# Performance work log

Hardware: AMD Instinct MI355X
Metric: run time of the kernel (lower is better)

Reference implementation:

```python
import jax, jax.numpy as jnp
import numpy as np

B, T, D, H, V = 512, 128, 1024, 1024, 256
STEPS = 26  # batch_max_length (25) + 1


def setup_inputs() -> dict:
    key = jax.random.key(0)
    ks = jax.random.split(key, 12)
    s = lambda *sh: 1.0 / np.sqrt(sh[-1])
    inp = {
        "batch_H": jax.random.normal(ks[0], (B, T, D), dtype=jnp.float32),
        "text": jax.random.randint(ks[1], (B, STEPS), 0, V, dtype=jnp.int64),
        # AttentionCell params
        "i2h_w": jax.random.normal(ks[2], (H, D), dtype=jnp.float32) * s(H, D),
        "h2h_w": jax.random.normal(ks[3], (H, H), dtype=jnp.float32) * s(H, H),
        "h2h_b": jnp.zeros((H,), dtype=jnp.float32),
        "score_w": jax.random.normal(ks[4], (1, H), dtype=jnp.float32) * s(1, H),
        # LSTMCell params (input = context[D] ++ onehot[V])
        "W_ih": jax.random.normal(ks[5], (4 * H, D + V), dtype=jnp.float32) * s(4 * H, D + V),
        "W_hh": jax.random.normal(ks[6], (4 * H, H), dtype=jnp.float32) * s(4 * H, H),
        "b_ih": jnp.zeros((4 * H,), dtype=jnp.float32),
        "b_hh": jnp.zeros((4 * H,), dtype=jnp.float32),
        # generator
        "gen_w": jax.random.normal(ks[7], (V, H), dtype=jnp.float32) * s(V, H),
        "gen_b": jnp.zeros((V,), dtype=jnp.float32),
    }
    return inp


def reference(batch_H, text, i2h_w, h2h_w, h2h_b, score_w, W_ih, W_hh, b_ih, b_hh, gen_w, gen_b):
    # proj_H = i2h(batch_H): step-invariant, hoisted out of the loop (same math)
    proj_H = jnp.einsum("btd,hd->bth", batch_H, i2h_w)  # [B,T,H]
    dtype = batch_H.dtype

    def step(carry, tok):
        h, c = carry
        # Bahdanau additive attention
        proj_h = h @ h2h_w.T + h2h_b                       # [B,H]
        e = jnp.tanh(proj_H + proj_h[:, None, :]) @ score_w[0]  # [B,T]
        alpha = jax.nn.softmax(e, axis=1)                   # [B,T]
        context = jnp.einsum("bt,btd->bd", alpha, batch_H)  # [B,D]
        x = jnp.concatenate([context, jax.nn.one_hot(tok, V, dtype=dtype)], axis=1)
        # LSTMCell (torch gate order: i, f, g, o)
        gates = x @ W_ih.T + b_ih + h @ W_hh.T + b_hh       # [B,4H]
        i_g, f_g, g_g, o_g = jnp.split(gates, 4, axis=1)
        c_new = jax.nn.sigmoid(f_g) * c + jax.nn.sigmoid(i_g) * jnp.tanh(g_g)
        h_new = jax.nn.sigmoid(o_g) * jnp.tanh(c_new)
        return (h_new, c_new), h_new

    h0 = jnp.zeros((B, H), dtype=dtype)
    c0 = jnp.zeros((B, H), dtype=dtype)
    tokens = jnp.swapaxes(text[:, :STEPS], 0, 1)            # [STEPS,B]
    _, out_hid = jax.lax.scan(step, (h0, c0), tokens)       # [STEPS,B,H]
    out_hid = jnp.swapaxes(out_hid, 0, 1)                   # [B,STEPS,H]
    logits = jnp.einsum("bsh,vh->bsv", out_hid, gen_w) + gen_b
    return logits  # [B, STEPS, V]
```

## Files before the change

### kernel.cpp

```cpp
#include <hip/hip_runtime.h>
#include <hip/hip_fp16.h>

#define BB 512
#define TT 128
#define DD 1024
#define HH 1024
#define VV 256
#define SS 26

typedef _Float16 half8 __attribute__((ext_vector_type(8)));
typedef _Float16 half4 __attribute__((ext_vector_type(4)));
typedef float f32x4 __attribute__((ext_vector_type(4)));

__device__ __forceinline__ float tanh_fast(float x) {
    float ex = __expf(2.f * x);
    return 1.f - 2.f * __builtin_amdgcn_rcpf(ex + 1.f);
}
__device__ __forceinline__ float sigmoid_fast(float x) {
    return __builtin_amdgcn_rcpf(1.f + __expf(-x));
}

__global__ void cvt_f32_to_f16_v4(const float* __restrict__ src,
                                  _Float16* __restrict__ dst, long n4) {
    long i = (long)blockIdx.x * blockDim.x + threadIdx.x;
    long stride = (long)gridDim.x * blockDim.x;
    for (; i < n4; i += stride) {
        float4 v = ((const float4*)src)[i];
        half4 h;
        h[0] = (_Float16)v.x; h[1] = (_Float16)v.y;
        h[2] = (_Float16)v.z; h[3] = (_Float16)v.w;
        ((half4*)dst)[i] = h;
    }
}

__global__ void build_wcatp(const float* __restrict__ W_ih,
                            const float* __restrict__ W_hh,
                            _Float16* __restrict__ wcatp) {
    int idx = blockIdx.x * 256 + threadIdx.x;
    int c = idx >> 11;
    int k = idx & 2047;
    int g = c >> 6, q = (c >> 4) & 3, jl = c & 15;
    int row = q * 1024 + g * 16 + jl;
    float v = (k < 1024) ? W_ih[(size_t)row * 1280 + k]
                         : W_hh[(size_t)row * 1024 + (k - 1024)];
    wcatp[idx] = (_Float16)v;
}

__global__ void build_onehT(const float* __restrict__ W_ih,
                            float* __restrict__ onehT) {
    int idx = blockIdx.x * 256 + threadIdx.x;
    int v = idx >> 12;
    int g = idx & 4095;
    onehT[idx] = W_ih[(size_t)g * 1280 + 1024 + v];
}

__global__ void build_bsum(const float* __restrict__ b_ih,
                           const float* __restrict__ b_hh,
                           float* __restrict__ bsum) {
    int i = blockIdx.x * 256 + threadIdx.x;
    bsum[i] = b_ih[i] + b_hh[i];
}

template <int MODE, int SWZ>
__global__ __launch_bounds__(256) void gemm_bt(
    const _Float16* __restrict__ A, int lda,
    const _Float16* __restrict__ B, int ldb,
    void* __restrict__ Cp, int ldc, int K, const float* __restrict__ bias) {
    __shared__ __align__(16) _Float16 As[128 * 32];
    __shared__ __align__(16) _Float16 Bs[128 * 32];

    int bx = blockIdx.x, by = blockIdx.y;
    if (SWZ) {
        int nx = gridDim.x;
        int bid = by * nx + bx;
        int xcd = bid & 7;
        int local = bid >> 3;
        int rows_per_xcd = gridDim.y >> 3;
        bx = local % nx;
        by = xcd * rows_per_xcd + local / nx;
    }
    const int tid  = threadIdx.x;
    const int lane = tid & 63;
    const int wid  = tid >> 6;
    const int wm   = wid >> 1;
    const int wn   = wid & 1;
    const int m0 = by * 128;
    const int n0 = bx * 128;

    f32x4 acc[4][4];
#pragma unroll
    for (int i = 0; i < 4; ++i)
#pragma unroll
        for (int j = 0; j < 4; ++j)
            acc[i][j] = (f32x4){0.f, 0.f, 0.f, 0.f};

    const int row0 = tid >> 2;
    const int ch0  = tid & 3;
    const _Float16* a0 = A + (size_t)(m0 + row0) * lda + ch0 * 8;
    const _Float16* a1 = A + (size_t)(m0 + row0 + 64) * lda + ch0 * 8;
    const _Float16* b0 = B + (size_t)(n0 + row0) * ldb + ch0 * 8;
    const _Float16* b1 = B + (size_t)(n0 + row0 + 64) * ldb + ch0 * 8;
    _Float16* sa0 = As + row0 * 32 + ch0 * 8;
    _Float16* sa1 = As + (row0 + 64) * 32 + ch0 * 8;
    _Float16* sb0 = Bs + row0 * 32 + ch0 * 8;
    _Float16* sb1 = Bs + (row0 + 64) * 32 + ch0 * 8;

    const int la = lane & 15;
    const int kc = (lane >> 4) * 8;

    for (int k0 = 0; k0 < K; k0 += 32) {
        uint4 va0 = *(const uint4*)(a0 + k0);
        uint4 va1 = *(const uint4*)(a1 + k0);
        uint4 vb0 = *(const uint4*)(b0 + k0);
        uint4 vb1 = *(const uint4*)(b1 + k0);
        __syncthreads();
        *(uint4*)sa0 = va0;
        *(uint4*)sa1 = va1;
        *(uint4*)sb0 = vb0;
        *(uint4*)sb1 = vb1;
        __syncthreads();

        half8 af[4], bf[4];
#pragma unroll
        for (int mt = 0; mt < 4; ++mt)
            af[mt] = *(const half8*)(As + (wm * 64 + mt * 16 + la) * 32 + kc);
#pragma unroll
        for (int nt = 0; nt < 4; ++nt)
            bf[nt] = *(const half8*)(Bs + (wn * 64 + nt * 16 + la) * 32 + kc);
#pragma unroll
        for (int mt = 0; mt < 4; ++mt)
#pragma unroll
            for (int nt = 0; nt < 4; ++nt)
                acc[mt][nt] = __builtin_amdgcn_mfma_f32_16x16x32_f16(
                    af[mt], bf[nt], acc[mt][nt], 0, 0, 0);
    }

#pragma unroll
    for (int mt = 0; mt < 4; ++mt) {
#pragma unroll
        for (int nt = 0; nt < 4; ++nt) {
            int gn = n0 + wn * 64 + nt * 16 + la;
            float bv = bias ? bias[gn] : 0.f;
#pragma unroll
            for (int r = 0; r < 4; ++r) {
                int gm = m0 + wm * 64 + mt * 16 + (lane >> 4) * 4 + r;
                float v = acc[mt][nt][r] + bv;
                if (MODE == 1) {
                    ((_Float16*)Cp)[(size_t)gm * ldc + gn] = (_Float16)v;
                } else {
                    int s = gm >> 9;
                    int b = gm & 511;
                    ((float*)Cp)[((size_t)b * SS + s) * VV + gn] = v;
                }
            }
        }
    }
}

#define GEMM64_CORE(A, lda, B, ldb, K)                                        \
    __shared__ __align__(16) _Float16 As[64 * 32];                            \
    __shared__ __align__(16) _Float16 Bs[128 * 32];                           \
    const int tid  = threadIdx.x;                                             \
    const int lane = tid & 63;                                                \
    const int wid  = tid >> 6;                                                \
    const int wm   = wid >> 1;                                                \
    const int wn   = wid & 1;                                                 \
    const int m0 = blockIdx.y * 64;                                           \
    const int n0 = blockIdx.x * 128;                                          \
    f32x4 acc[2][4];                                                          \
    _Pragma("unroll") for (int i = 0; i < 2; ++i)                             \
        _Pragma("unroll") for (int j = 0; j < 4; ++j)                         \
            acc[i][j] = (f32x4){0.f, 0.f, 0.f, 0.f};                          \
    const int row0 = tid >> 2;                                                \
    const int ch0  = tid & 3;                                                 \
    const _Float16* ag = A + (size_t)(m0 + row0) * lda + ch0 * 8;             \
    const _Float16* bg0 = B + (size_t)(n0 + row0) * ldb + ch0 * 8;            \
    const _Float16* bg1 = B + (size_t)(n0 + row0 + 64) * ldb + ch0 * 8;       \
    _Float16* sa  = As + row0 * 32 + ch0 * 8;                                 \
    _Float16* sb0 = Bs + row0 * 32 + ch0 * 8;                                 \
    _Float16* sb1 = Bs + (row0 + 64) * 32 + ch0 * 8;                          \
    const int la = lane & 15;                                                 \
    const int kc = (lane >> 4) * 8;                                           \
    for (int k0 = 0; k0 < K; k0 += 32) {                                      \
        uint4 va  = *(const uint4*)(ag + k0);                                 \
        uint4 vb0 = *(const uint4*)(bg0 + k0);                                \
        uint4 vb1 = *(const uint4*)(bg1 + k0);                                \
        __syncthreads();                                                      \
        *(uint4*)sa  = va;                                                    \
        *(uint4*)sb0 = vb0;                                                   \
        *(uint4*)sb1 = vb1;                                                   \
        __syncthreads();                                                      \
        half8 af[2], bf[4];                                                   \
        _Pragma("unroll") for (int mt = 0; mt < 2; ++mt)                      \
            af[mt] = *(const half8*)(As + (wm * 32 + mt * 16 + la) * 32 + kc);\
        _Pragma("unroll") for (int nt = 0; nt < 4; ++nt)                      \
            bf[nt] = *(const half8*)(Bs + (wn * 64 + nt * 16 + la) * 32 + kc);\
        _Pragma("unroll") for (int mt = 0; mt < 2; ++mt)                      \
            _Pragma("unroll") for (int nt = 0; nt < 4; ++nt)                  \
                acc[mt][nt] = __builtin_amdgcn_mfma_f32_16x16x32_f16(         \
                    af[mt], bf[nt], acc[mt][nt], 0, 0, 0);                    \
    }

__global__ __launch_bounds__(256) void gemm64_f32(
    const _Float16* __restrict__ A, int lda,
    const _Float16* __restrict__ B, int ldb,
    float* __restrict__ C, int ldc, int K, const float* __restrict__ bias) {
    GEMM64_CORE(A, lda, B, ldb, K)
#pragma unroll
    for (int mt = 0; mt < 2; ++mt)
#pragma unroll
        for (int nt = 0; nt < 4; ++nt) {
            int gn = n0 + wn * 64 + nt * 16 + la;
            float bv = bias[gn];
#pragma unroll
            for (int r = 0; r < 4; ++r) {
                int gm = m0 + wm * 32 + mt * 16 + (lane >> 4) * 4 + r;
                C[(size_t)gm * ldc + gn] = acc[mt][nt][r] + bv;
            }
        }
}

__global__ __launch_bounds__(256) void gemm_gates(
    const _Float16* __restrict__ A,
    const _Float16* __restrict__ B,
    const float* __restrict__ bsum,
    const float* __restrict__ onehT,
    const int* __restrict__ text,
    int step,
    float* __restrict__ c,
    _Float16* __restrict__ acat,
    _Float16* __restrict__ hid) {
    GEMM64_CORE(A, 2048, B, 2048, 2048)
    const int quad = lane >> 4;
    const int jb = (n0 >> 2) + wn * 16 + la;
    float bs[4];
#pragma unroll
    for (int q = 0; q < 4; ++q) bs[q] = bsum[q * 1024 + jb];
#pragma unroll
    for (int mt = 0; mt < 2; ++mt) {
#pragma unroll
        for (int r = 0; r < 4; ++r) {
            int b = m0 + wm * 32 + mt * 16 + quad * 4 + r;
            int tok = text[b * SS + step];
            const float* orow = onehT + (size_t)tok * 4096;
            float ig = acc[mt][0][r] + bs[0] + orow[jb];
            float fg = acc[mt][1][r] + bs[1] + orow[1024 + jb];
            float gg = acc[mt][2][r] + bs[2] + orow[2048 + jb];
            float og = acc[mt][3][r] + bs[3] + orow[3072 + jb];
            size_t ci = (size_t)b * 1024 + jb;
            float cn = sigmoid_fast(fg) * c[ci] + sigmoid_fast(ig) * tanh_fast(gg);
            float hn = sigmoid_fast(og) * tanh_fast(cn);
            c[ci] = cn;
            _Float16 h16 = (_Float16)hn;
            acat[(size_t)b * 2048 + 1024 + jb] = h16;
            hid[((size_t)step * BB + b) * HH + jb] = h16;
        }
    }
}

__global__ __launch_bounds__(256) void attn_kernel(
    const _Float16* __restrict__ pH,
    const _Float16* __restrict__ bh,
    const float* __restrict__ ph,
    const float* __restrict__ sw,
    _Float16* __restrict__ acat) {
    __shared__ float e_s[TT];
    __shared__ float al_s[TT];

    const int b = blockIdx.x;
    const int tid = threadIdx.x;
    const int lane = tid & 63;
    const int wv = tid >> 6;

    float phr[16], swr[16];
    const float4* ph4 = (const float4*)(ph + (size_t)b * HH + lane * 16);
    const float4* sw4 = (const float4*)(sw + lane * 16);
#pragma unroll
    for (int q = 0; q < 4; ++q) {
        float4 t1 = ph4[q];
        phr[q * 4 + 0] = t1.x; phr[q * 4 + 1] = t1.y;
        phr[q * 4 + 2] = t1.z; phr[q * 4 + 3] = t1.w;
        float4 t2 = sw4[q];
        swr[q * 4 + 0] = t2.x; swr[q * 4 + 1] = t2.y;
        swr[q * 4 + 2] = t2.z; swr[q * 4 + 3] = t2.w;
    }

    const _Float16* pHb = pH + (size_t)b * TT * HH + lane * 16;
    for (int tt = 0; tt < 32; ++tt) {
        int t = wv * 32 + tt;
        half8 p0 = *(const half8*)(pHb + (size_t)t * HH);
        half8 p1 = *(const half8*)(pHb + (size_t)t * HH + 8);
        float acc = 0.f;
#pragma unroll
        for (int k = 0; k < 8; ++k)
            acc += tanh_fast((float)p0[k] + phr[k]) * swr[k];
#pragma unroll
        for (int k = 0; k < 8; ++k)
            acc += tanh_fast((float)p1[k] + phr[8 + k]) * swr[8 + k];
#pragma unroll
        for (int off = 32; off > 0; off >>= 1) acc += __shfl_xor(acc, off, 64);
        if (lane == 0) e_s[t] = acc;
    }
    __syncthreads();

    if (tid < TT) {
        float m = -1e30f;
        for (int t = 0; t < TT; ++t) m = fmaxf(m, e_s[t]);
        float s = 0.f;
        for (int t = 0; t < TT; ++t) s += __expf(e_s[t] - m);
        al_s[tid] = __expf(e_s[tid] - m) / s;
    }
    __syncthreads();

    const _Float16* bhb = bh + (size_t)b * TT * DD + tid * 4;
    float c0 = 0.f, c1 = 0.f, c2 = 0.f, c3 = 0.f;
#pragma unroll 4
    for (int t = 0; t < TT; ++t) {
        float a = al_s[t];
        half4 v = *(const half4*)(bhb + (size_t)t * DD);
        c0 += a * (float)v[0];
        c1 += a * (float)v[1];
        c2 += a * (float)v[2];
        c3 += a * (float)v[3];
    }
    half4 o;
    o[0] = (_Float16)c0; o[1] = (_Float16)c1;
    o[2] = (_Float16)c2; o[3] = (_Float16)c3;
    *(half4*)(acat + (size_t)b * 2048 + tid * 4) = o;
}

extern "C" void kernel_launch(void* const* d_in, const int* in_sizes, int n_in,
                              void* d_out, int out_size, void* d_ws, size_t ws_size,
                              hipStream_t stream) {
    const float* batch_H = (const float*)d_in[0];
    const int*   text    = (const int*)d_in[1];
    const float* i2h_w   = (const float*)d_in[2];
    const float* h2h_w   = (const float*)d_in[3];
    const float* h2h_b   = (const float*)d_in[4];
    const float* score_w = (const float*)d_in[5];
    const float* W_ih    = (const float*)d_in[6];
    const float* W_hh    = (const float*)d_in[7];
    const float* b_ih    = (const float*)d_in[8];
    const float* b_hh    = (const float*)d_in[9];
    const float* gen_w   = (const float*)d_in[10];
    const float* gen_b   = (const float*)d_in[11];
    float* out = (float*)d_out;

    char* ws = (char*)d_ws;
    size_t off = 0;
    auto carve = [&](size_t bytes) -> void* {
        void* p = ws + off;
        off += (bytes + 255) & ~(size_t)255;
        return p;
    };
    _Float16* bh16   = (_Float16*)carve((size_t)BB * TT * DD * 2);
    _Float16* pH16   = (_Float16*)carve((size_t)BB * TT * HH * 2);
    _Float16* wi2h16 = (_Float16*)carve((size_t)HH * DD * 2);
    _Float16* wh2h16 = (_Float16*)carve((size_t)HH * HH * 2);
    _Float16* wcatp  = (_Float16*)carve((size_t)4 * HH * 2048 * 2);
    _Float16* wgen16 = (_Float16*)carve((size_t)VV * HH * 2);
    float*    onehT  = (float*)carve((size_t)VV * 4 * HH * 4);
    float*    bsum   = (float*)carve((size_t)4 * HH * 4);
    _Float16* acat   = (_Float16*)carve((size_t)BB * 2048 * 2);
    float*    ph_f   = (float*)carve((size_t)BB * HH * 4);
    float*    c_f    = (float*)carve((size_t)BB * HH * 4);
    _Float16* hid16  = (_Float16*)carve((size_t)SS * BB * HH * 2);

    const dim3 blk(256);

    cvt_f32_to_f16_v4<<<dim3(16384), blk, 0, stream>>>(batch_H, bh16, (long)BB * TT * DD / 4);
    cvt_f32_to_f16_v4<<<dim3(1024), blk, 0, stream>>>(i2h_w, wi2h16, (long)HH * DD / 4);
    cvt_f32_to_f16_v4<<<dim3(1024), blk, 0, stream>>>(h2h_w, wh2h16, (long)HH * HH / 4);
    cvt_f32_to_f16_v4<<<dim3(256), blk, 0, stream>>>(gen_w, wgen16, (long)VV * HH / 4);
    build_wcatp<<<dim3(4 * HH * 2048 / 256), blk, 0, stream>>>(W_ih, W_hh, wcatp);
    build_onehT<<<dim3(VV * 4 * HH / 256), blk, 0, stream>>>(W_ih, onehT);
    build_bsum<<<dim3(16), blk, 0, stream>>>(b_ih, b_hh, bsum);
    hipMemsetAsync(acat, 0, (size_t)BB * 2048 * 2, stream);
    hipMemsetAsync(c_f, 0, (size_t)BB * HH * 4, stream);

    gemm_bt<1, 1><<<dim3(HH / 128, BB * TT / 128), blk, 0, stream>>>(
        bh16, DD, wi2h16, DD, pH16, HH, DD, nullptr);

    for (int s = 0; s < SS; ++s) {
        gemm64_f32<<<dim3(HH / 128, BB / 64), blk, 0, stream>>>(
            acat + 1024, 2048, wh2h16, HH, ph_f, HH, HH, h2h_b);

        attn_kernel<<<dim3(BB), blk, 0, stream>>>(pH16, bh16, ph_f, score_w, acat);

        gemm_gates<<<dim3(4 * HH / 128, BB / 64), blk, 0, stream>>>(
            acat, wcatp, bsum, onehT, text, s, c_f, acat, hid16);
    }

    gemm_bt<2, 0><<<dim3(VV / 128, SS * BB / 128), blk, 0, stream>>>(
        hid16, HH, wgen16, HH, out, VV, HH, gen_b);
}
```

Measured before the change: 3.920 ms.

## Use direct global-to-LDS loads in GEMMs and widen attention to 512 threads

```diff
diff --git a/kernel.cpp b/kernel.cpp
--- a/kernel.cpp
+++ b/kernel.cpp
@@ -11,6 +11,12 @@
 typedef _Float16 half8 __attribute__((ext_vector_type(8)));
 typedef _Float16 half4 __attribute__((ext_vector_type(4)));
 typedef float f32x4 __attribute__((ext_vector_type(4)));
+
+__device__ __forceinline__ void cp16(const void* g, void* l) {
+    __builtin_amdgcn_global_load_lds(
+        (const __attribute__((address_space(1))) void*)g,
+        (__attribute__((address_space(3))) void*)l, 16, 0, 0);
+}
 
 __device__ __forceinline__ float tanh_fast(float x) {
     float ex = __expf(2.f * x);
@@ -100,24 +106,20 @@
     const _Float16* a1 = A + (size_t)(m0 + row0 + 64) * lda + ch0 * 8;
     const _Float16* b0 = B + (size_t)(n0 + row0) * ldb + ch0 * 8;
     const _Float16* b1 = B + (size_t)(n0 + row0 + 64) * ldb + ch0 * 8;
-    _Float16* sa0 = As + row0 * 32 + ch0 * 8;
-    _Float16* sa1 = As + (row0 + 64) * 32 + ch0 * 8;
-    _Float16* sb0 = Bs + row0 * 32 + ch0 * 8;
-    _Float16* sb1 = Bs + (row0 + 64) * 32 + ch0 * 8;
+    _Float16* sa0 = As + tid * 8;
+    _Float16* sa1 = As + 64 * 32 + tid * 8;
+    _Float16* sb0 = Bs + tid * 8;
+    _Float16* sb1 = Bs + 64 * 32 + tid * 8;
 
     const int la = lane & 15;
     const int kc = (lane >> 4) * 8;
 
     for (int k0 = 0; k0 < K; k0 += 32) {
-        uint4 va0 = *(const uint4*)(a0 + k0);
-        uint4 va1 = *(const uint4*)(a1 + k0);
-        uint4 vb0 = *(const uint4*)(b0 + k0);
-        uint4 vb1 = *(const uint4*)(b1 + k0);
         __syncthreads();
-        *(uint4*)sa0 = va0;
-        *(uint4*)sa1 = va1;
-        *(uint4*)sb0 = vb0;
-        *(uint4*)sb1 = vb1;
+        cp16(a0 + k0, sa0);
+        cp16(a1 + k0, sa1);
+        cp16(b0 + k0, sb0);
+        cp16(b1 + k0, sb1);
         __syncthreads();
 
         half8 af[4], bf[4];
@@ -173,22 +175,19 @@
             acc[i][j] = (f32x4){0.f, 0.f, 0.f, 0.f};                          \
     const int row0 = tid >> 2;                                                \
     const int ch0  = tid & 3;                                                 \
-    const _Float16* ag = A + (size_t)(m0 + row0) * lda + ch0 * 8;             \
+    const _Float16* ag  = A + (size_t)(m0 + row0) * lda + ch0 * 8;            \
     const _Float16* bg0 = B + (size_t)(n0 + row0) * ldb + ch0 * 8;            \
     const _Float16* bg1 = B + (size_t)(n0 + row0 + 64) * ldb + ch0 * 8;       \
-    _Float16* sa  = As + row0 * 32 + ch0 * 8;                                 \
-    _Float16* sb0 = Bs + row0 * 32 + ch0 * 8;                                 \
-    _Float16* sb1 = Bs + (row0 + 64) * 32 + ch0 * 8;                          \
+    _Float16* sa  = As + tid * 8;                                             \
+    _Float16* sb0 = Bs + tid * 8;                                             \
+    _Float16* sb1 = Bs + 64 * 32 + tid * 8;                                   \
     const int la = lane & 15;                                                 \
     const int kc = (lane >> 4) * 8;                                           \
     for (int k0 = 0; k0 < K; k0 += 32) {                                      \
-        uint4 va  = *(const uint4*)(ag + k0);                                 \
-        uint4 vb0 = *(const uint4*)(bg0 + k0);                                \
-        uint4 vb1 = *(const uint4*)(bg1 + k0);                                \
         __syncthreads();                                                      \
-        *(uint4*)sa  = va;                                                    \
-        *(uint4*)sb0 = vb0;                                                   \
-        *(uint4*)sb1 = vb1;                                                   \
+        cp16(ag + k0, sa);                                                    \
+        cp16(bg0 + k0, sb0);                                                  \
+        cp16(bg1 + k0, sb1);                                                  \
         __syncthreads();                                                      \
         half8 af[2], bf[4];                                                   \
         _Pragma("unroll") for (int mt = 0; mt < 2; ++mt)                      \
@@ -258,7 +257,7 @@
     }
 }
 
-__global__ __launch_bounds__(256) void attn_kernel(
+__global__ __launch_bounds__(512) void attn_kernel(
     const _Float16* __restrict__ pH,
     const _Float16* __restrict__ bh,
     const float* __restrict__ ph,
@@ -266,6 +265,7 @@
     _Float16* __restrict__ acat) {
     __shared__ float e_s[TT];
     __shared__ float al_s[TT];
+    __shared__ __align__(16) float pc[2][DD];
 
     const int b = blockIdx.x;
     const int tid = threadIdx.x;
@@ -286,8 +286,8 @@
     }
 
     const _Float16* pHb = pH + (size_t)b * TT * HH + lane * 16;
-    for (int tt = 0; tt < 32; ++tt) {
-        int t = wv * 32 + tt;
+    for (int tt = 0; tt < 16; ++tt) {
+        int t = wv * 16 + tt;
         half8 p0 = *(const half8*)(pHb + (size_t)t * HH);
         half8 p1 = *(const half8*)(pHb + (size_t)t * HH + 8);
         float acc = 0.f;
@@ -312,10 +312,12 @@
     }
     __syncthreads();
 
-    const _Float16* bhb = bh + (size_t)b * TT * DD + tid * 4;
+    const int w2 = tid >> 8;
+    const int lc = tid & 255;
+    const _Float16* bhb = bh + (size_t)b * TT * DD + lc * 4;
     float c0 = 0.f, c1 = 0.f, c2 = 0.f, c3 = 0.f;
 #pragma unroll 4
-    for (int t = 0; t < TT; ++t) {
+    for (int t = w2 * 64; t < w2 * 64 + 64; ++t) {
         float a = al_s[t];
         half4 v = *(const half4*)(bhb + (size_t)t * DD);
         c0 += a * (float)v[0];
@@ -323,10 +325,19 @@
         c2 += a * (float)v[2];
         c3 += a * (float)v[3];
     }
-    half4 o;
-    o[0] = (_Float16)c0; o[1] = (_Float16)c1;
-    o[2] = (_Float16)c2; o[3] = (_Float16)c3;
-    *(half4*)(acat + (size_t)b * 2048 + tid * 4) = o;
+    ((float4*)pc[w2])[lc] = make_float4(c0, c1, c2, c3);
+    __syncthreads();
+
+    if (tid < 256) {
+        float4 x0 = ((const float4*)pc[0])[tid];
+        float4 x1 = ((const float4*)pc[1])[tid];
+        half4 o;
+        o[0] = (_Float16)(x0.x + x1.x);
+        o[1] = (_Float16)(x0.y + x1.y);
+        o[2] = (_Float16)(x0.z + x1.z);
+        o[3] = (_Float16)(x0.w + x1.w);
+        *(half4*)(acat + (size_t)b * 2048 + tid * 4) = o;
+    }
 }
 
 extern "C" void kernel_launch(void* const* d_in, const int* in_sizes, int n_in,
@@ -385,7 +396,7 @@
         gemm64_f32<<<dim3(HH / 128, BB / 64), blk, 0, stream>>>(
             acat + 1024, 2048, wh2h16, HH, ph_f, HH, HH, h2h_b);
 
-        attn_kernel<<<dim3(BB), blk, 0, stream>>>(pH16, bh16, ph_f, score_w, acat);
+        attn_kernel<<<dim3(BB), dim3(512), 0, stream>>>(pH16, bh16, ph_f, score_w, acat);
 
         gemm_gates<<<dim3(4 * HH / 128, BB / 64), blk, 0, stream>>>(
             acat, wcatp, bsum, onehT, text, s, c_f, acat, hid16);
```

Measured after the change: 3.582 ms. -8.6%, faster.
